# Kernel optimization log

Measured on AMD Instinct MI355X. Metric: run time of the kernel, lower is better.

Reference implementation:

```python
import jax, jax.numpy as jnp
import numpy as np

N_NODES = 100000
N_EDGES = 1600000
IN_CH = 128
HID = 128
OUT_CH = 10
NUM_LAYERS = 3
NUM_GRAPHS = 512


def _glorot(key, shape):
    fan_in, fan_out = shape[0], shape[1]
    lim = jnp.sqrt(6.0 / (fan_in + fan_out))
    return jax.random.uniform(key, shape, jnp.float32, -lim, lim)


def setup_inputs() -> dict:
    key = jax.random.key(0)
    ks = jax.random.split(key, 20)
    inp = {}
    inp["x"] = jax.random.normal(ks[0], (N_NODES, IN_CH), jnp.float32)
    inp["edge_index"] = jax.random.randint(ks[1], (2, N_EDGES), 0, N_NODES, jnp.int64)
    inp["batch"] = jnp.sort(jax.random.randint(ks[2], (N_NODES,), 0, NUM_GRAPHS, jnp.int64))
    # GIN layer MLP params: Linear(in, hid) -> ReLU -> Linear(hid, hid)
    kidx = 3
    for l in range(NUM_LAYERS):
        d_in = IN_CH if l == 0 else HID
        inp[f"w1_{l}"] = _glorot(ks[kidx], (d_in, HID)); kidx += 1
        inp[f"b1_{l}"] = jnp.zeros((HID,), jnp.float32)
        inp[f"w2_{l}"] = _glorot(ks[kidx], (HID, HID)); kidx += 1
        inp[f"b2_{l}"] = jnp.zeros((HID,), jnp.float32)
    inp["lin_w"] = _glorot(ks[kidx], (HID, OUT_CH))
    inp["lin_b"] = jnp.zeros((OUT_CH,), jnp.float32)
    return inp


def _gin_forward(x, src, dst, batch, layer_params, lin_w, lin_b):
    h = x
    n_layers = len(layer_params)
    for i, (w1, b1, w2, b2) in enumerate(layer_params):
        # GINConv: (1 + eps) * h + sum_{j in N(i)} h_j, eps = 0
        agg = jax.ops.segment_sum(h[src], dst, num_segments=N_NODES)
        z = h + agg
        # MLP: Linear -> ReLU -> Linear
        h = jnp.maximum(z @ w1 + b1, 0.0) @ w2 + b2
        if i < n_layers - 1:  # inter-layer ReLU (PyG BasicGNN act)
            h = jnp.maximum(h, 0.0)
    # global_add_pool over batch ids -> [NUM_GRAPHS, HID]
    pooled = jax.ops.segment_sum(h, batch, num_segments=NUM_GRAPHS)
    # dropout(p=0.5) is identity in eval mode
    return pooled @ lin_w + lin_b


def reference(x, edge_index, batch,
              w1_0, b1_0, w2_0, b2_0,
              w1_1, b1_1, w2_1, b2_1,
              w1_2, b1_2, w2_2, b2_2,
              lin_w, lin_b):
    src, dst = edge_index[0], edge_index[1]
    layer_params = [(w1_0, b1_0, w2_0, b2_0),
                    (w1_1, b1_1, w2_1, b2_1),
                    (w1_2, b1_2, w2_2, b2_2)]
    return _gin_forward(x, src, dst, batch, layer_params, lin_w, lin_b)
```

## Files before the change

kernel.cpp:

```cpp
#include <hip/hip_runtime.h>

#define CH 128
#define OUTC 10
#define NB 256
#define BCAP 10240
#define PCHUNK 2048
#define PQ2 132
#define FBM 64

typedef __attribute__((ext_vector_type(8))) short short8;
typedef __attribute__((ext_vector_type(4))) short short4v;
typedef __attribute__((ext_vector_type(16))) float f32x16;
typedef __attribute__((ext_vector_type(2))) float f32x2;


__device__ inline unsigned short f2bf(float f) {
    unsigned u = __builtin_bit_cast(unsigned, f);
    u += 0x7fffu + ((u >> 16) & 1u);
    return (unsigned short)(u >> 16);
}
__device__ inline float bflo(unsigned u) { return __builtin_bit_cast(float, u << 16); }
__device__ inline float bfhi(unsigned u) { return __builtin_bit_cast(float, u & 0xffff0000u); }

__device__ inline f32x2 bf2(unsigned u) {
    return (f32x2){__builtin_bit_cast(float, u << 16),
                   __builtin_bit_cast(float, u & 0xffff0000u)};
}

__device__ inline void acc8(f32x2* a, const uint4& v) {
    a[0] += bf2(v.x);
    a[1] += bf2(v.y);
    a[2] += bf2(v.z);
    a[3] += bf2(v.w);
}


struct WPtrs { const float* s[6]; unsigned short* d[6]; };

__global__ void prep_part_kernel(const int* __restrict__ src, const int* __restrict__ dst,
                                 int* __restrict__ bucketCnt, unsigned* __restrict__ pairs, int E,
                                 int nPartBlk,
                                 const float4* __restrict__ x4, uint2* __restrict__ xb, int n4,
                                 int nConvBlk, WPtrs p,
                                 uint4* __restrict__ pooled4, int nPooled4) {
    __shared__ int hist[NB];
    __shared__ int base[NB];
    __shared__ int cur[NB];
    int tid = threadIdx.x;
    int b = blockIdx.x;

    if (b < nPartBlk) {
        int e0 = b * PCHUNK;
        hist[tid] = 0;
        __syncthreads();
        #pragma unroll
        for (int i = 0; i < PCHUNK / 256; ++i) {
            int e = e0 + tid + i * 256;
            if (e < E) atomicAdd(&hist[dst[e] >> 9], 1);
        }
        __syncthreads();
        {
            int c = hist[tid];
            base[tid] = (c > 0) ? atomicAdd(&bucketCnt[tid], c) : 0;
            cur[tid] = 0;
        }
        __syncthreads();
        #pragma unroll
        for (int i = 0; i < PCHUNK / 256; ++i) {
            int e = e0 + tid + i * 256;
            if (e < E) {
                int d = dst[e];
                int bkt = d >> 9;
                int pos = base[bkt] + atomicAdd(&cur[bkt], 1);
                if (pos < BCAP)
                    pairs[bkt * BCAP + pos] = ((unsigned)(d & 511) << 17) | (unsigned)src[e];
            }
        }
    } else if (b < nPartBlk + nConvBlk) {
        int i = (b - nPartBlk) * 256 + tid;
        if (i < n4) {
            float4 v = x4[i];
            uint2 o;
            o.x = (unsigned)f2bf(v.x) | ((unsigned)f2bf(v.y) << 16);
            o.y = (unsigned)f2bf(v.z) | ((unsigned)f2bf(v.w) << 16);
            xb[i] = o;
        }
    } else if (b < nPartBlk + nConvBlk + 384) {
        int bb = b - nPartBlk - nConvBlk;
        int m = bb >> 6;
        int i = (bb & 63) * 256 + tid;
        int j = i & 7;
        int l = (i >> 3) & 63;
        int k0 = (i >> 9) & 7;
        int ct = (i >> 12) & 3;
        int k = k0 * 16 + ((l >> 5) << 3) + j;
        int nn = ct * 32 + (l & 31);
        p.d[m][i] = f2bf(p.s[m][k * CH + nn]);
    } else {
        int i = (b - nPartBlk - nConvBlk - 384) * 256 + tid;
        if (i < nPooled4) pooled4[i] = make_uint4(0, 0, 0, 0);
    }
}


__launch_bounds__(512)
__global__ void build_csr_kernel(const unsigned* __restrict__ pairs, const int* __restrict__ bucketCnt,
                                 int* __restrict__ offs, int* __restrict__ csr, int N) {
    __shared__ int bsm[NB];
    __shared__ int ldeg[512];
    __shared__ int s0[512], s1[512];
    __shared__ int lexc[512];
    __shared__ int lcur[512];
    __shared__ int lcsr[BCAP];

    int b = blockIdx.x;
    int node0 = b << 9;
    if (node0 >= N) return;
    int nLocal = min(512, N - node0);
    int tid = threadIdx.x;

    if (tid < NB) bsm[tid] = bucketCnt[tid];
    __syncthreads();
    for (int off = 1; off < NB; off <<= 1) {
        int t = 0;
        if (tid < NB) t = (tid >= off) ? bsm[tid - off] : 0;
        __syncthreads();
        if (tid < NB) bsm[tid] += t;
        __syncthreads();
    }
    int cnt = min(bucketCnt[b], BCAP);
    int gbase = bsm[b] - bucketCnt[b];

    ldeg[tid] = 0;
    __syncthreads();
    for (int i = tid; i < cnt; i += 512)
        atomicAdd(&ldeg[pairs[b * BCAP + i] >> 17], 1);
    __syncthreads();

    s0[tid] = ldeg[tid];
    __syncthreads();
    int* sp = s0; int* dp = s1;
    for (int off = 1; off < 512; off <<= 1) {
        dp[tid] = sp[tid] + ((tid >= off) ? sp[tid - off] : 0);
        __syncthreads();
        int* t = sp; sp = dp; dp = t;
    }
    {
        int ex = sp[tid] - ldeg[tid];
        lexc[tid] = ex;
        lcur[tid] = ex;
    }
    __syncthreads();

    for (int i = tid; i < cnt; i += 512) {
        unsigned w = pairs[b * BCAP + i];
        int ppos = atomicAdd(&lcur[w >> 17], 1);
        lcsr[ppos] = (int)(w & 0x1ffffu);
    }
    __syncthreads();

    for (int i = tid; i < cnt; i += 512) csr[gbase + i] = lcsr[i];
    for (int i = tid; i < nLocal; i += 512) offs[node0 + i] = gbase + lexc[i];
    if (tid == 0 && node0 + nLocal == N) offs[N] = gbase + cnt;
}


template <int L, int RELU, int POOL>
__launch_bounds__(512)
__global__ void fused_gin_kernel(const uint4* __restrict__ h4,
                                 const int* __restrict__ offs, const int* __restrict__ csr,
                                 const unsigned short* __restrict__ w1s, const float* __restrict__ b1,
                                 const unsigned short* __restrict__ w2s, const float* __restrict__ b2,
                                 unsigned short* __restrict__ hout,
                                 const int* __restrict__ batch, float* __restrict__ pooled,
                                 int n) {
    __shared__ __align__(16) unsigned short zs[FBM * PQ2];

    int tid = threadIdx.x;
    int row0 = blockIdx.x * FBM;

    {
        int gl = tid & 15;
        int grp = tid >> 4;
        #pragma unroll
        for (int it = 0; it < 2; ++it) {
            int rr = grp + 32 * it;
            int node = row0 + rr;
            unsigned o0 = 0, o1 = 0, o2 = 0, o3 = 0;
            if (node < n) {
                int beg = offs[node], end = offs[node + 1];
                f32x2 a[4];
                uint4 self = h4[node * 16 + gl];
                a[0] = bf2(self.x);
                a[1] = bf2(self.y);
                a[2] = bf2(self.z);
                a[3] = bf2(self.w);
                int e = beg;
                int elim = beg + ((end - beg) & ~3);
                if (e < elim) {
                    int s0 = csr[e], s1 = csr[e + 1], s2 = csr[e + 2], s3 = csr[e + 3];
                    for (; e + 8 <= elim; e += 4) {
                        uint4 v0 = h4[s0 * 16 + gl];
                        uint4 v1 = h4[s1 * 16 + gl];
                        uint4 v2 = h4[s2 * 16 + gl];
                        uint4 v3 = h4[s3 * 16 + gl];
                        int t0 = csr[e + 4], t1 = csr[e + 5], t2 = csr[e + 6], t3 = csr[e + 7];
                        acc8(a, v0); acc8(a, v1); acc8(a, v2); acc8(a, v3);
                        s0 = t0; s1 = t1; s2 = t2; s3 = t3;
                    }
                    {
                        uint4 v0 = h4[s0 * 16 + gl];
                        uint4 v1 = h4[s1 * 16 + gl];
                        uint4 v2 = h4[s2 * 16 + gl];
                        uint4 v3 = h4[s3 * 16 + gl];
                        acc8(a, v0); acc8(a, v1); acc8(a, v2); acc8(a, v3);
                        e += 4;
                    }
                }
                for (; e < end; ++e) {
                    uint4 v = h4[csr[e] * 16 + gl];
                    acc8(a, v);
                }
                o0 = (unsigned)f2bf(a[0][0]) | ((unsigned)f2bf(a[0][1]) << 16);
                o1 = (unsigned)f2bf(a[1][0]) | ((unsigned)f2bf(a[1][1]) << 16);
                o2 = (unsigned)f2bf(a[2][0]) | ((unsigned)f2bf(a[2][1]) << 16);
                o3 = (unsigned)f2bf(a[3][0]) | ((unsigned)f2bf(a[3][1]) << 16);
            }
            *(uint2*)&zs[rr * PQ2 + gl * 8]     = make_uint2(o0, o1);
            *(uint2*)&zs[rr * PQ2 + gl * 8 + 4] = make_uint2(o2, o3);
        }
    }
    __syncthreads();

    int wv = tid >> 6;
    int lane = tid & 63;
    int l31 = lane & 31;
    int kh = lane >> 5;
    int rt = wv & 1;
    int ct = wv >> 1;
    int arow = rt * 32 + l31;

    f32x16 acc;
    {
        float bv = b1[ct * 32 + l31];
        #pragma unroll
        for (int r = 0; r < 16; ++r) acc[r] = bv;
    }
    #pragma unroll
    for (int k0 = 0; k0 < 8; ++k0) {
        short8 afr;
        {
            short4v lo = *(const short4v*)&zs[arow * PQ2 + k0 * 16 + kh * 8];
            short4v hi = *(const short4v*)&zs[arow * PQ2 + k0 * 16 + kh * 8 + 4];
            afr = (short8){lo[0], lo[1], lo[2], lo[3], hi[0], hi[1], hi[2], hi[3]};
        }
        short8 bfr = *(const short8*)&w1s[(((ct * 8 + k0) * 64) + lane) * 8];
        acc = __builtin_amdgcn_mfma_f32_32x32x16_bf16(afr, bfr, acc, 0, 0, 0);
    }
    __syncthreads();

    #pragma unroll
    for (int reg = 0; reg < 16; ++reg) {
        int crow = (reg & 3) + 8 * (reg >> 2) + 4 * kh;
        zs[(rt * 32 + crow) * PQ2 + ct * 32 + l31] = f2bf(fmaxf(acc[reg], 0.f));
    }
    __syncthreads();

    {
        float bv = b2[ct * 32 + l31];
        #pragma unroll
        for (int r = 0; r < 16; ++r) acc[r] = bv;
    }
    #pragma unroll
    for (int k0 = 0; k0 < 8; ++k0) {
        short8 afr;
        {
            short4v lo = *(const short4v*)&zs[arow * PQ2 + k0 * 16 + kh * 8];
            short4v hi = *(const short4v*)&zs[arow * PQ2 + k0 * 16 + kh * 8 + 4];
            afr = (short8){lo[0], lo[1], lo[2], lo[3], hi[0], hi[1], hi[2], hi[3]};
        }
        short8 bfr = *(const short8*)&w2s[(((ct * 8 + k0) * 64) + lane) * 8];
        acc = __builtin_amdgcn_mfma_f32_32x32x16_bf16(afr, bfr, acc, 0, 0, 0);
    }
    __syncthreads();

    #pragma unroll
    for (int reg = 0; reg < 16; ++reg) {
        int crow = (reg & 3) + 8 * (reg >> 2) + 4 * kh;
        float v = acc[reg];
        if (RELU) v = fmaxf(v, 0.f);
        zs[(rt * 32 + crow) * PQ2 + ct * 32 + l31] = f2bf(v);
    }
    __syncthreads();

    if (!POOL) {
        for (int i = tid; i < FBM * 16; i += 512) {
            int r = i >> 4, c = i & 15;
            int row = row0 + r;
            if (row < n) {
                uint2 a2 = *(const uint2*)&zs[r * PQ2 + c * 8];
                uint2 b2v = *(const uint2*)&zs[r * PQ2 + c * 8 + 4];
                ((uint4*)hout)[row * 16 + c] = make_uint4(a2.x, a2.y, b2v.x, b2v.y);
            }
        }
    } else {
        int c2 = tid & 63;
        int rs = tid >> 6;
        float a0 = 0.f, a1 = 0.f;
        int prevg = -1;
        #pragma unroll
        for (int i = 0; i < FBM / 8; ++i) {
            int r = rs + 8 * i;
            int row = row0 + r;
            if (row >= n) break;
            int g = batch[row];
            if (g != prevg) {
                if (prevg >= 0) {
                    atomicAdd(&pooled[prevg * CH + 2 * c2], a0);
                    atomicAdd(&pooled[prevg * CH + 2 * c2 + 1], a1);
                }
                prevg = g; a0 = 0.f; a1 = 0.f;
            }
            unsigned v = *(const unsigned*)&zs[r * PQ2 + c2 * 2];
            a0 += bflo(v); a1 += bfhi(v);
        }
        if (prevg >= 0) {
            atomicAdd(&pooled[prevg * CH + 2 * c2], a0);
            atomicAdd(&pooled[prevg * CH + 2 * c2 + 1], a1);
        }
    }
}


__global__ void final_linear_kernel(const float* __restrict__ pooled, const float* __restrict__ lin_w,
                                    const float* __restrict__ lin_b, float* __restrict__ out) {
    int g = blockIdx.x;
    int tid = threadIdx.x;
    __shared__ float pl[CH];
    pl[tid] = pooled[g * CH + tid];
    __syncthreads();
    if (tid < OUTC) {
        float a = lin_b[tid];
        #pragma unroll 16
        for (int c = 0; c < CH; ++c) a = fmaf(pl[c], lin_w[c * OUTC + tid], a);
        out[g * OUTC + tid] = a;
    }
}


static inline size_t aln(size_t x) { return (x + 255) & ~size_t(255); }

extern "C" void kernel_launch(void* const* d_in, const int* in_sizes, int n_in,
                              void* d_out, int out_size, void* d_ws, size_t ws_size,
                              hipStream_t stream) {
    const float* x      = (const float*)d_in[0];
    const int*   ei     = (const int*)d_in[1];
    const int*   batch  = (const int*)d_in[2];
    const float* w1[3]  = {(const float*)d_in[3], (const float*)d_in[7],  (const float*)d_in[11]};
    const float* b1[3]  = {(const float*)d_in[4], (const float*)d_in[8],  (const float*)d_in[12]};
    const float* w2[3]  = {(const float*)d_in[5], (const float*)d_in[9],  (const float*)d_in[13]};
    const float* b2[3]  = {(const float*)d_in[6], (const float*)d_in[10], (const float*)d_in[14]};
    const float* lin_w  = (const float*)d_in[15];
    const float* lin_b  = (const float*)d_in[16];
    float* out = (float*)d_out;

    int E = in_sizes[1] / 2;
    int N = in_sizes[2];
    int n_graphs = out_size / OUTC;
    const int* src = ei;
    const int* dst = ei + E;

    char* p = (char*)d_ws;
    int* bucketCnt  = (int*)p; p += aln(NB * 4);
    unsigned* pairs = (unsigned*)p; p += aln((size_t)NB * BCAP * 4);
    int* offs       = (int*)p; p += aln((size_t)(N + 1) * 4);
    int* csr        = (int*)p; p += aln((size_t)E * 4);
    unsigned short* xb = (unsigned short*)p; p += aln((size_t)N * CH * 2);
    unsigned short* hA = (unsigned short*)p; p += aln((size_t)N * CH * 2);
    unsigned short* hB = (unsigned short*)p; p += aln((size_t)N * CH * 2);
    float* pooled = (float*)p; p += aln((size_t)n_graphs * CH * 4);
    unsigned short* wt[6];
    for (int i = 0; i < 6; ++i) { wt[i] = (unsigned short*)p; p += aln((size_t)CH * CH * 2); }
    (void)ws_size; (void)n_in;

    hipMemsetAsync(bucketCnt, 0, NB * 4, stream);

    int n4 = N * CH / 4;
    int nConvBlk = (n4 + 255) / 256;
    int nPartBlk = (E + PCHUNK - 1) / PCHUNK;
    int nPooled4 = n_graphs * CH / 4;
    int nZeroBlk = (nPooled4 + 255) / 256;
    WPtrs wp;
    for (int l = 0; l < 3; ++l) {
        wp.s[2 * l] = w1[l];     wp.d[2 * l] = wt[2 * l];
        wp.s[2 * l + 1] = w2[l]; wp.d[2 * l + 1] = wt[2 * l + 1];
    }
    prep_part_kernel<<<nPartBlk + nConvBlk + 384 + nZeroBlk, 256, 0, stream>>>(
        src, dst, bucketCnt, pairs, E, nPartBlk,
        (const float4*)x, (uint2*)xb, n4, nConvBlk, wp,
        (uint4*)pooled, nPooled4);

    build_csr_kernel<<<NB, 512, 0, stream>>>(pairs, bucketCnt, offs, csr, N);

    int fblk = (N + FBM - 1) / FBM;

    fused_gin_kernel<0, 1, 0><<<fblk, 512, 0, stream>>>((const uint4*)xb, offs, csr,
        wt[0], b1[0], wt[1], b2[0], hA, batch, pooled, N);
    fused_gin_kernel<1, 1, 0><<<fblk, 512, 0, stream>>>((const uint4*)hA, offs, csr,
        wt[2], b1[1], wt[3], b2[1], hB, batch, pooled, N);
    fused_gin_kernel<2, 0, 1><<<fblk, 512, 0, stream>>>((const uint4*)hB, offs, csr,
        wt[4], b1[2], wt[5], b2[2], (unsigned short*)nullptr, batch, pooled, N);

    final_linear_kernel<<<n_graphs, CH, 0, stream>>>(pooled, lin_w, lin_b, out);
}
```

Baseline: 372.9 us.

## Degree-balance node assignment in fused GIN gather via per-tile sorted permutation

The CSR build kernel now sorts each 64-node tile by in-degree with an odd-even transposition sort and writes a permutation. The two 32-node halves of each wave pair high-degree nodes with low-degree ones. The fused GIN kernel gathers nodes through this permutation so lanes in a wave have more similar total neighbor counts, which is meant to reduce divergence stalls in the gather loop. The software-pipelined csr prefetch in the gather loop is also replaced by a simpler 4-wide loop. The cost is a 64-round sort with barriers in the build kernel and an extra perm load per node.

```diff
diff --git a/kernel.cpp b/kernel.cpp
--- a/kernel.cpp
+++ b/kernel.cpp
@@ -105,12 +105,14 @@
 
 __launch_bounds__(512)
 __global__ void build_csr_kernel(const unsigned* __restrict__ pairs, const int* __restrict__ bucketCnt,
-                                 int* __restrict__ offs, int* __restrict__ csr, int N) {
+                                 int* __restrict__ offs, int* __restrict__ csr,
+                                 int* __restrict__ perm, int N) {
     __shared__ int bsm[NB];
     __shared__ int ldeg[512];
     __shared__ int s0[512], s1[512];
     __shared__ int lexc[512];
     __shared__ int lcur[512];
+    __shared__ int skey[512];
     __shared__ int lcsr[BCAP];
 
     int b = blockIdx.x;
@@ -162,6 +164,25 @@
     for (int i = tid; i < cnt; i += 512) csr[gbase + i] = lcsr[i];
     for (int i = tid; i < nLocal; i += 512) offs[node0 + i] = gbase + lexc[i];
     if (tid == 0 && node0 + nLocal == N) offs[N] = gbase + cnt;
+
+    skey[tid] = (ldeg[tid] << 6) | (tid & 63);
+    __syncthreads();
+    for (int r = 0; r < 64; ++r) {
+        int i = tid & 63;
+        int s = tid & ~63;
+        if (((i & 1) == (r & 1)) && (i + 1 < 64)) {
+            int a = skey[s + i], c = skey[s + i + 1];
+            if (a < c) { skey[s + i] = c; skey[s + i + 1] = a; }
+        }
+        __syncthreads();
+    }
+    {
+        int i = tid & 63;
+        int s = tid & ~63;
+        int rank = (i < 32) ? i : (95 - i);
+        int loc = skey[s + rank] & 63;
+        perm[node0 + s + i] = node0 + s + loc;
+    }
 }
 
 
@@ -169,6 +190,7 @@
 __launch_bounds__(512)
 __global__ void fused_gin_kernel(const uint4* __restrict__ h4,
                                  const int* __restrict__ offs, const int* __restrict__ csr,
+                                 const int* __restrict__ perm,
                                  const unsigned short* __restrict__ w1s, const float* __restrict__ b1,
                                  const unsigned short* __restrict__ w2s, const float* __restrict__ b2,
                                  unsigned short* __restrict__ hout,
@@ -182,10 +204,13 @@
     {
         int gl = tid & 15;
         int grp = tid >> 4;
+        int pbase = blockIdx.x << 6;
+        int nodeA = perm[pbase + grp];
+        int nodeB = perm[pbase + 32 + grp];
         #pragma unroll
         for (int it = 0; it < 2; ++it) {
-            int rr = grp + 32 * it;
-            int node = row0 + rr;
+            int node = it ? nodeB : nodeA;
+            int rr = node - row0;
             unsigned o0 = 0, o1 = 0, o2 = 0, o3 = 0;
             if (node < n) {
                 int beg = offs[node], end = offs[node + 1];
@@ -196,26 +221,13 @@
                 a[2] = bf2(self.z);
                 a[3] = bf2(self.w);
                 int e = beg;
-                int elim = beg + ((end - beg) & ~3);
-                if (e < elim) {
+                for (; e + 4 <= end; e += 4) {
                     int s0 = csr[e], s1 = csr[e + 1], s2 = csr[e + 2], s3 = csr[e + 3];
-                    for (; e + 8 <= elim; e += 4) {
-                        uint4 v0 = h4[s0 * 16 + gl];
-                        uint4 v1 = h4[s1 * 16 + gl];
-                        uint4 v2 = h4[s2 * 16 + gl];
-                        uint4 v3 = h4[s3 * 16 + gl];
-                        int t0 = csr[e + 4], t1 = csr[e + 5], t2 = csr[e + 6], t3 = csr[e + 7];
-                        acc8(a, v0); acc8(a, v1); acc8(a, v2); acc8(a, v3);
-                        s0 = t0; s1 = t1; s2 = t2; s3 = t3;
-                    }
-                    {
-                        uint4 v0 = h4[s0 * 16 + gl];
-                        uint4 v1 = h4[s1 * 16 + gl];
-                        uint4 v2 = h4[s2 * 16 + gl];
-                        uint4 v3 = h4[s3 * 16 + gl];
-                        acc8(a, v0); acc8(a, v1); acc8(a, v2); acc8(a, v3);
-                        e += 4;
-                    }
+                    uint4 v0 = h4[s0 * 16 + gl];
+                    uint4 v1 = h4[s1 * 16 + gl];
+                    uint4 v2 = h4[s2 * 16 + gl];
+                    uint4 v3 = h4[s3 * 16 + gl];
+                    acc8(a, v0); acc8(a, v1); acc8(a, v2); acc8(a, v3);
                 }
                 for (; e < end; ++e) {
                     uint4 v = h4[csr[e] * 16 + gl];
@@ -375,6 +387,7 @@
     unsigned* pairs = (unsigned*)p; p += aln((size_t)NB * BCAP * 4);
     int* offs       = (int*)p; p += aln((size_t)(N + 1) * 4);
     int* csr        = (int*)p; p += aln((size_t)E * 4);
+    int* perm       = (int*)p; p += aln((size_t)((N + 511) & ~511) * 4);
     unsigned short* xb = (unsigned short*)p; p += aln((size_t)N * CH * 2);
     unsigned short* hA = (unsigned short*)p; p += aln((size_t)N * CH * 2);
     unsigned short* hB = (unsigned short*)p; p += aln((size_t)N * CH * 2);
@@ -400,15 +413,15 @@
         (const float4*)x, (uint2*)xb, n4, nConvBlk, wp,
         (uint4*)pooled, nPooled4);
 
-    build_csr_kernel<<<NB, 512, 0, stream>>>(pairs, bucketCnt, offs, csr, N);
+    build_csr_kernel<<<NB, 512, 0, stream>>>(pairs, bucketCnt, offs, csr, perm, N);
 
     int fblk = (N + FBM - 1) / FBM;
 
-    fused_gin_kernel<0, 1, 0><<<fblk, 512, 0, stream>>>((const uint4*)xb, offs, csr,
+    fused_gin_kernel<0, 1, 0><<<fblk, 512, 0, stream>>>((const uint4*)xb, offs, csr, perm,
         wt[0], b1[0], wt[1], b2[0], hA, batch, pooled, N);
-    fused_gin_kernel<1, 1, 0><<<fblk, 512, 0, stream>>>((const uint4*)hA, offs, csr,
+    fused_gin_kernel<1, 1, 0><<<fblk, 512, 0, stream>>>((const uint4*)hA, offs, csr, perm,
         wt[2], b1[1], wt[3], b2[1], hB, batch, pooled, N);
-    fused_gin_kernel<2, 0, 1><<<fblk, 512, 0, stream>>>((const uint4*)hB, offs, csr,
+    fused_gin_kernel<2, 0, 1><<<fblk, 512, 0, stream>>>((const uint4*)hB, offs, csr, perm,
         wt[4], b1[2], wt[5], b2[2], (unsigned short*)nullptr, batch, pooled, N);
 
     final_linear_kernel<<<n_graphs, CH, 0, stream>>>(pooled, lin_w, lin_b, out);
```

Measured after the change: 384.3 us. 1.03x slower.
